# Optimization experiments

Measured on AMD Instinct MI355X. Metric: run time of the kernel, lower is better.

## Reference

```python
import jax, jax.numpy as jnp
import numpy as np

B, S, D, H = 4, 2048, 1024, 16
HD = D // H

def setup_inputs() -> dict:
    key = jax.random.key(0)
    k1, k2, k3, k4, k5 = jax.random.split(key, 5)
    sc = 1.0 / np.sqrt(D)
    return {
        "x": jax.random.normal(k1, (B, S, D), dtype=jnp.float32),
        "w_qkv": jax.random.normal(k2, (D, 3 * D), dtype=jnp.float32) * sc,
        "b_qkv": jnp.zeros((3 * D,), dtype=jnp.float32),
        "w_proj": jax.random.normal(k3, (D, D), dtype=jnp.float32) * sc,
        "b_proj": jnp.zeros((D,), dtype=jnp.float32),
    }

def reference(x, w_qkv, b_qkv, w_proj, b_proj):
    bsz, seq_len, dim = x.shape
    qkv = x @ w_qkv + b_qkv                      # [B,S,3D]
    q, k, v = jnp.split(qkv, 3, axis=2)
    q = q.reshape(bsz, seq_len, H, HD).transpose(0, 2, 1, 3)  # [B,H,S,hd]
    k = k.reshape(bsz, seq_len, H, HD).transpose(0, 2, 1, 3)
    v = v.reshape(bsz, seq_len, H, HD).transpose(0, 2, 1, 3)
    att = jnp.einsum('bhqd,bhkd->bhqk', q, k) * (1.0 / np.sqrt(HD))
    causal = jnp.tril(jnp.ones((seq_len, seq_len), dtype=bool))
    att = jnp.where(causal[None, None], att, -jnp.inf)
    att = jax.nn.softmax(att, axis=-1)
    y = jnp.einsum('bhqk,bhkd->bhqd', att, v)
    y = y.transpose(0, 2, 1, 3).reshape(bsz, seq_len, dim)
    return y @ w_proj + b_proj
```

## Files before the change

kernel.cpp:

```cpp
#include <hip/hip_runtime.h>
#include <cstdint>
#include <cstddef>

typedef float  f32x4  __attribute__((ext_vector_type(4)));
typedef __bf16 bf16x8 __attribute__((ext_vector_type(8)));
typedef __bf16 bf16x4 __attribute__((ext_vector_type(4)));

#define DEVI static __device__ __forceinline__

DEVI f32x4 mfma_bf16(bf16x8 a, bf16x8 b, f32x4 c) {
  return __builtin_amdgcn_mfma_f32_16x16x32_bf16(a, b, c, 0, 0, 0);
}

DEVI void gload_lds16(const void* g, void* l) {
  __builtin_amdgcn_global_load_lds(
      (const __attribute__((address_space(1))) void*)g,
      (__attribute__((address_space(3))) void*)l, 16, 0, 0);
}

__global__ void k_cast_bf16(const float* __restrict__ src, __bf16* __restrict__ dst, int n4) {
  int i = blockIdx.x * blockDim.x + threadIdx.x;
  if (i < n4) {
    float4 v = reinterpret_cast<const float4*>(src)[i];
    bf16x4 r;
    r.x = (__bf16)v.x; r.y = (__bf16)v.y; r.z = (__bf16)v.z; r.w = (__bf16)v.w;
    reinterpret_cast<bf16x4*>(dst)[i] = r;
  }
}

__global__ void k_transpose_cast(const float* __restrict__ src, __bf16* __restrict__ dst,
                                 int R, int C) {
  __shared__ __bf16 tile[64][65];
  const int tx = threadIdx.x & 63, ty = threadIdx.x >> 6;
  const int r0 = blockIdx.y * 64, c0 = blockIdx.x * 64;
#pragma unroll
  for (int i = 0; i < 16; ++i) {
    int r = ty * 16 + i;
    tile[r][tx] = (__bf16)src[(size_t)(r0 + r) * C + c0 + tx];
  }
  __syncthreads();
#pragma unroll
  for (int i = 0; i < 16; ++i) {
    int c = ty * 16 + i;
    dst[(size_t)(c0 + c) * R + r0 + tx] = tile[tx][c];
  }
}

__global__ void k_transpose_v(const __bf16* __restrict__ qkv, __bf16* __restrict__ VT) {
  __shared__ __bf16 tile[64][65];
  const int tx = threadIdx.x & 63, ty = threadIdx.x >> 6;
  const int bh = blockIdx.y;
  const int b = bh >> 4, h = bh & 15;
  const int s0 = blockIdx.x * 64;
  const __bf16* src = qkv + (size_t)(b * 2048) * 3072 + 2048 + h * 64;
#pragma unroll
  for (int i = 0; i < 16; ++i) {
    int s = ty * 16 + i;
    tile[s][tx] = src[(size_t)(s0 + s) * 3072 + tx];
  }
  __syncthreads();
  __bf16* dst = VT + (size_t)bh * 64 * 2048;
#pragma unroll
  for (int i = 0; i < 16; ++i) {
    int d = ty * 16 + i;
    dst[(size_t)d * 2048 + s0 + tx] = tile[tx][d];
  }
}

template <int MODE>
__global__ __launch_bounds__(256, 2) void k_gemm_bt(
    const __bf16* __restrict__ A, const __bf16* __restrict__ Bt,
    const float* __restrict__ bias, void* __restrict__ Cv,
    int M, int N, int K, int nbx) {
  __shared__ __bf16 As[128 * 64];
  __shared__ __bf16 Bs[128 * 64];
  const int t = threadIdx.x;
  const int w = t >> 6, lane = t & 63;
  const int l15 = lane & 15, lg = lane >> 4;
  const int m0 = (blockIdx.x / nbx) * 128;
  const int n0 = (blockIdx.x % nbx) * 128;
  const int wr = w >> 1, wc = w & 1;
  const int lrow = lane >> 3, lslot = lane & 7;

  f32x4 acc[4][4] = {};

  const int nK = K >> 6;
  for (int kt = 0; kt < nK; ++kt) {
    const __bf16* Ab = A + (size_t)m0 * K + kt * 64;
    const __bf16* Bb = Bt + (size_t)n0 * K + kt * 64;
#pragma unroll
    for (int c = 0; c < 4; ++c) {
      int seg = w * 4 + c;
      int row = seg * 8 + lrow;
      int cb = (lslot ^ (row & 7)) << 4;
      gload_lds16((const char*)(Ab + (size_t)row * K) + cb, (char*)As + seg * 1024);
      gload_lds16((const char*)(Bb + (size_t)row * K) + cb, (char*)Bs + seg * 1024);
    }
    __syncthreads();
#pragma unroll
    for (int ks = 0; ks < 2; ++ks) {
      bf16x8 af[4], bfr[4];
      const int cb = ks * 64 + (lg << 4);
#pragma unroll
      for (int m = 0; m < 4; ++m) {
        int row = wr * 64 + m * 16 + l15;
        af[m] = *(const bf16x8*)((const char*)As + row * 128 + (cb ^ ((row & 7) << 4)));
      }
#pragma unroll
      for (int n = 0; n < 4; ++n) {
        int row = wc * 64 + n * 16 + l15;
        bfr[n] = *(const bf16x8*)((const char*)Bs + row * 128 + (cb ^ ((row & 7) << 4)));
      }
#pragma unroll
      for (int m = 0; m < 4; ++m)
#pragma unroll
        for (int n = 0; n < 4; ++n)
          acc[m][n] = mfma_bf16(af[m], bfr[n], acc[m][n]);
    }
    __syncthreads();
  }

#pragma unroll
  for (int n = 0; n < 4; ++n) {
    const int gcol = n0 + wc * 64 + n * 16 + l15;
    const float bv = bias ? bias[gcol] : 0.0f;
#pragma unroll
    for (int m = 0; m < 4; ++m) {
      const int grow = m0 + wr * 64 + m * 16 + (lg << 2);
#pragma unroll
      for (int r = 0; r < 4; ++r) {
        float v = acc[m][n][r] + bv;
        if (MODE == 0)
          ((__bf16*)Cv)[(size_t)(grow + r) * N + gcol] = (__bf16)v;
        else
          ((float*)Cv)[(size_t)(grow + r) * N + gcol] = v;
      }
    }
  }
}

__global__ __launch_bounds__(512, 2) void k_attn(
    const __bf16* __restrict__ qkv,
    const __bf16* __restrict__ VT,
    __bf16* __restrict__ Y) {
  __shared__ __bf16 kbuf[2][64 * 64];
  __shared__ __bf16 vbuf[2][64 * 64];
  __shared__ __bf16 p_lds[8][1024];
  const int t = threadIdx.x, w = t >> 6, lane = t & 63;
  const int l15 = lane & 15, lg = lane >> 4;
  const int bid = blockIdx.x;
  const int qt = 15 - (bid >> 6);
  const int bh = bid & 63;
  const int b = bh >> 4, h = bh & 15;
  const int q0 = qt * 128;
  const int nkv = 2 * qt + 2;
  const float SCL = 0.125f * 1.44269504f;

  const size_t qrow = (size_t)(b * 2048 + q0 + w * 16 + l15);
  const bf16x8 qf0 = *(const bf16x8*)(qkv + qrow * 3072 + h * 64 + lg * 8);
  const bf16x8 qf1 = *(const bf16x8*)(qkv + qrow * 3072 + h * 64 + 32 + lg * 8);

  const __bf16* kg = qkv + (size_t)(b * 2048) * 3072 + 1024 + h * 64;
  const __bf16* vg = VT + (size_t)bh * 64 * 2048;

  const int srow = t >> 3, sslot = t & 7;
  const int sb = (sslot ^ (srow & 7)) << 4;
  auto stage = [&](int bi, int kvi) {
    gload_lds16((const char*)(kg + (size_t)(kvi * 64 + srow) * 3072) + sb,
                (char*)kbuf[bi] + w * 1024);
    gload_lds16((const char*)(vg + (size_t)srow * 2048 + kvi * 64) + sb,
                (char*)vbuf[bi] + w * 1024);
  };

  f32x4 o[4] = {};
  float mr = -1e30f, lr = 0.0f;
  __bf16* pl = &p_lds[w][0];

  stage(0, 0);
  asm volatile("s_waitcnt vmcnt(0)" ::: "memory");
  __syncthreads();

  for (int kv = 0; kv < nkv; ++kv) {
    if (kv + 1 < nkv) stage((kv + 1) & 1, kv + 1);
    const char* kb = (const char*)kbuf[kv & 1];
    const char* vb = (const char*)vbuf[kv & 1];

    f32x4 s[4] = {};
    __builtin_amdgcn_s_setprio(1);
#pragma unroll
    for (int nb = 0; nb < 4; ++nb) {
      int row = nb * 16 + l15;
      int sw = (row & 7) << 4;
      bf16x8 k0 = *(const bf16x8*)(kb + row * 128 + ((lg * 16) ^ sw));
      bf16x8 k1 = *(const bf16x8*)(kb + row * 128 + ((64 + lg * 16) ^ sw));
      s[nb] = mfma_bf16(k0, qf0, s[nb]);
      s[nb] = mfma_bf16(k1, qf1, s[nb]);
    }
    __builtin_amdgcn_s_setprio(0);

    if (((kv + 1) << 6) > q0 + w * 16) {
      const int qg = q0 + w * 16 + l15;
#pragma unroll
      for (int nb = 0; nb < 4; ++nb)
#pragma unroll
        for (int r = 0; r < 4; ++r)
          if (kv * 64 + nb * 16 + lg * 4 + r > qg) s[nb][r] = -1e30f;
    }

    float pm = -3e38f;
#pragma unroll
    for (int nb = 0; nb < 4; ++nb)
      pm = fmaxf(pm, fmaxf(fmaxf(s[nb][0], s[nb][1]), fmaxf(s[nb][2], s[nb][3])));
    pm = fmaxf(pm, __shfl_xor(pm, 16));
    pm = fmaxf(pm, __shfl_xor(pm, 32));
    pm *= SCL;

    if (!__all(pm <= mr + 8.0f)) {
      float nm = fmaxf(mr, pm);
      float alpha = __builtin_amdgcn_exp2f(mr - nm);
      lr *= alpha;
      mr = nm;
#pragma unroll
      for (int r = 0; r < 4; ++r) {
        float aO = __shfl(alpha, lg * 4 + r);
        o[0][r] *= aO; o[1][r] *= aO; o[2][r] *= aO; o[3][r] *= aO;
      }
    }

    float ps = 0.0f;
    bf16x4 pk[4];
#pragma unroll
    for (int nb = 0; nb < 4; ++nb) {
      f32x4 pe;
#pragma unroll
      for (int r = 0; r < 4; ++r)
        pe[r] = __builtin_amdgcn_exp2f(fmaf(s[nb][r], SCL, -mr));
      ps += (pe[0] + pe[1]) + (pe[2] + pe[3]);
      pk[nb][0] = (__bf16)pe[0]; pk[nb][1] = (__bf16)pe[1];
      pk[nb][2] = (__bf16)pe[2]; pk[nb][3] = (__bf16)pe[3];
    }
    ps += __shfl_xor(ps, 16);
    ps += __shfl_xor(ps, 32);
    lr += ps;

    {
      const int rowb = l15 * 128;
      const int sw = (l15 & 7) << 4;
#pragma unroll
      for (int nb = 0; nb < 4; ++nb) {
        int cb = (nb * 32 + lg * 8) ^ sw;
        *(bf16x4*)((char*)pl + rowb + cb) = pk[nb];
      }
    }
    asm volatile("s_waitcnt lgkmcnt(0)" ::: "memory");
    bf16x8 pf0, pf1;
    {
      const int rowb = l15 * 128;
      const int sw = (l15 & 7) << 4;
      pf0 = *(const bf16x8*)((const char*)pl + rowb + ((lg << 4) ^ sw));
      pf1 = *(const bf16x8*)((const char*)pl + rowb + ((64 + (lg << 4)) ^ sw));
    }
    __builtin_amdgcn_s_setprio(1);
#pragma unroll
    for (int nb = 0; nb < 4; ++nb) {
      int row = nb * 16 + l15;
      int sw = (row & 7) << 4;
      bf16x8 v0 = *(const bf16x8*)(vb + row * 128 + ((lg * 16) ^ sw));
      bf16x8 v1 = *(const bf16x8*)(vb + row * 128 + ((64 + lg * 16) ^ sw));
      o[nb] = mfma_bf16(pf0, v0, o[nb]);
      o[nb] = mfma_bf16(pf1, v1, o[nb]);
    }
    __builtin_amdgcn_s_setprio(0);
    asm volatile("s_waitcnt vmcnt(0)" ::: "memory");
    __syncthreads();
  }

  float lO[4];
#pragma unroll
  for (int r = 0; r < 4; ++r) lO[r] = __shfl(lr, lg * 4 + r);
#pragma unroll
  for (int nb = 0; nb < 4; ++nb)
#pragma unroll
    for (int r = 0; r < 4; ++r) {
      float v = o[nb][r] / lO[r];
      size_t row = (size_t)(b * 2048 + q0 + w * 16 + lg * 4 + r);
      Y[row * 1024 + h * 64 + nb * 16 + l15] = (__bf16)v;
    }
}

extern "C" void kernel_launch(void* const* d_in, const int* in_sizes, int n_in,
                              void* d_out, int out_size, void* d_ws, size_t ws_size,
                              hipStream_t stream) {
  const float* x      = (const float*)d_in[0];
  const float* w_qkv  = (const float*)d_in[1];
  const float* b_qkv  = (const float*)d_in[2];
  const float* w_proj = (const float*)d_in[3];
  const float* b_proj = (const float*)d_in[4];
  float* out = (float*)d_out;

  char* ws = (char*)d_ws;
  const size_t MB = 1024 * 1024;
  __bf16* xb     = (__bf16*)(ws);
  __bf16* wqkvT  = (__bf16*)(ws + 16 * MB);
  __bf16* wprojT = (__bf16*)(ws + 22 * MB);
  __bf16* qkv    = (__bf16*)(ws + 24 * MB);
  __bf16* VT     = (__bf16*)(ws + 72 * MB);
  __bf16* Y      = (__bf16*)(ws + 88 * MB);

  k_cast_bf16<<<8192, 256, 0, stream>>>(x, xb, 8192 * 1024 / 4);
  k_transpose_cast<<<dim3(48, 16), 256, 0, stream>>>(w_qkv, wqkvT, 1024, 3072);
  k_transpose_cast<<<dim3(16, 16), 256, 0, stream>>>(w_proj, wprojT, 1024, 1024);
  k_gemm_bt<0><<<dim3(64 * 24), 256, 0, stream>>>(xb, wqkvT, b_qkv, qkv, 8192, 3072, 1024, 24);
  k_transpose_v<<<dim3(32, 64), 256, 0, stream>>>(qkv, VT);
  k_attn<<<dim3(1024), 512, 0, stream>>>(qkv, VT, Y);
  k_gemm_bt<1><<<dim3(64 * 8), 256, 0, stream>>>(Y, wprojT, b_proj, out, 8192, 1024, 1024, 8);
}
```

Measured before the change: 178.2 us.

## Replace GEMM with 256x256-tile, 8-wave, double-buffered pipelined kernel

```diff
diff --git a/kernel.cpp b/kernel.cpp
--- a/kernel.cpp
+++ b/kernel.cpp
@@ -68,56 +68,127 @@
 }
 
 template <int MODE>
-__global__ __launch_bounds__(256, 2) void k_gemm_bt(
+__global__ __launch_bounds__(512, 2) void k_gemm8(
     const __bf16* __restrict__ A, const __bf16* __restrict__ Bt,
     const float* __restrict__ bias, void* __restrict__ Cv,
     int M, int N, int K, int nbx) {
-  __shared__ __bf16 As[128 * 64];
-  __shared__ __bf16 Bs[128 * 64];
+  __shared__ alignas(16) __bf16 Asl[2][2][256 * 32];
+  __shared__ alignas(16) __bf16 Bsl[2][2][256 * 32];
   const int t = threadIdx.x;
   const int w = t >> 6, lane = t & 63;
   const int l15 = lane & 15, lg = lane >> 4;
-  const int m0 = (blockIdx.x / nbx) * 128;
-  const int n0 = (blockIdx.x % nbx) * 128;
-  const int wr = w >> 1, wc = w & 1;
-  const int lrow = lane >> 3, lslot = lane & 7;
-
-  f32x4 acc[4][4] = {};
-
+  const int wr = w >> 2, wc = w & 3;
+
+  const int nwg = gridDim.x;
+  const int wgid = (blockIdx.x & 7) * (nwg >> 3) + (blockIdx.x >> 3);
+  const int m0 = (wgid / nbx) * 256;
+  const int n0 = (wgid % nbx) * 256;
+
+  const int lrow = lane & 15, lcol = lane >> 4;
+  const __bf16* pa = A + (size_t)(m0 + lrow) * K + lcol * 8;
+  const __bf16* pb = Bt + (size_t)(n0 + lrow) * K + lcol * 8;
+
+  auto stageA = [&](int buf, int kt, int kk) {
+    const __bf16* src = pa + (size_t)kt * 64 + kk * 32;
+    char* dst = (char*)&Asl[buf][kk][0];
+#pragma unroll
+    for (int i = 0; i < 2; ++i) {
+      const int st = w * 2 + i;
+      gload_lds16(src + (size_t)st * 16 * K, dst + st * 1024);
+    }
+  };
+  auto stageB = [&](int buf, int kt, int kk) {
+    const __bf16* src = pb + (size_t)kt * 64 + kk * 32;
+    char* dst = (char*)&Bsl[buf][kk][0];
+#pragma unroll
+    for (int i = 0; i < 2; ++i) {
+      const int st = w * 2 + i;
+      gload_lds16(src + (size_t)st * 16 * K, dst + st * 1024);
+    }
+  };
+
+  const int aoff = wr * 8192 + lg * 256 + l15 * 16;
+  const int boff = wc * 4096 + lg * 256 + l15 * 16;
+
+  f32x4 acc[8][4] = {};
   const int nK = K >> 6;
+
+  stageA(0, 0, 0); stageB(0, 0, 0);
+  stageA(0, 0, 1); stageB(0, 0, 1);
+  asm volatile("s_waitcnt vmcnt(4)" ::: "memory");
+  __builtin_amdgcn_s_barrier();
+
   for (int kt = 0; kt < nK; ++kt) {
-    const __bf16* Ab = A + (size_t)m0 * K + kt * 64;
-    const __bf16* Bb = Bt + (size_t)n0 * K + kt * 64;
-#pragma unroll
-    for (int c = 0; c < 4; ++c) {
-      int seg = w * 4 + c;
-      int row = seg * 8 + lrow;
-      int cb = (lslot ^ (row & 7)) << 4;
-      gload_lds16((const char*)(Ab + (size_t)row * K) + cb, (char*)As + seg * 1024);
-      gload_lds16((const char*)(Bb + (size_t)row * K) + cb, (char*)Bs + seg * 1024);
-    }
-    __syncthreads();
-#pragma unroll
-    for (int ks = 0; ks < 2; ++ks) {
-      bf16x8 af[4], bfr[4];
-      const int cb = ks * 64 + (lg << 4);
-#pragma unroll
-      for (int m = 0; m < 4; ++m) {
-        int row = wr * 64 + m * 16 + l15;
-        af[m] = *(const bf16x8*)((const char*)As + row * 128 + (cb ^ ((row & 7) << 4)));
-      }
-#pragma unroll
-      for (int n = 0; n < 4; ++n) {
-        int row = wc * 64 + n * 16 + l15;
-        bfr[n] = *(const bf16x8*)((const char*)Bs + row * 128 + (cb ^ ((row & 7) << 4)));
-      }
-#pragma unroll
-      for (int m = 0; m < 4; ++m)
-#pragma unroll
-        for (int n = 0; n < 4; ++n)
-          acc[m][n] = mfma_bf16(af[m], bfr[n], acc[m][n]);
-    }
-    __syncthreads();
+    const int buf = kt & 1, nbuf = buf ^ 1;
+    const bool pf = (kt + 1) < nK;
+    const char* a0 = (const char*)&Asl[buf][0][0];
+    const char* b0 = (const char*)&Bsl[buf][0][0];
+    const char* a1 = (const char*)&Asl[buf][1][0];
+    const char* b1 = (const char*)&Bsl[buf][1][0];
+    bf16x8 af[4], bfr[4];
+
+#pragma unroll
+    for (int m = 0; m < 4; ++m) af[m] = *(const bf16x8*)(a0 + aoff + m * 1024);
+#pragma unroll
+    for (int n = 0; n < 4; ++n) bfr[n] = *(const bf16x8*)(b0 + boff + n * 1024);
+    if (pf) stageA(nbuf, kt + 1, 0);
+    __builtin_amdgcn_s_barrier();
+    asm volatile("s_waitcnt lgkmcnt(0)" ::: "memory");
+    __builtin_amdgcn_s_setprio(1);
+#pragma unroll
+    for (int m = 0; m < 4; ++m)
+#pragma unroll
+      for (int n = 0; n < 4; ++n)
+        acc[m][n] = mfma_bf16(af[m], bfr[n], acc[m][n]);
+    __builtin_amdgcn_s_setprio(0);
+    __builtin_amdgcn_s_barrier();
+
+#pragma unroll
+    for (int m = 0; m < 4; ++m) af[m] = *(const bf16x8*)(a0 + aoff + (m + 4) * 1024);
+    if (pf) stageB(nbuf, kt + 1, 0);
+    __builtin_amdgcn_s_barrier();
+    asm volatile("s_waitcnt lgkmcnt(0)" ::: "memory");
+    __builtin_amdgcn_s_setprio(1);
+#pragma unroll
+    for (int m = 0; m < 4; ++m)
+#pragma unroll
+      for (int n = 0; n < 4; ++n)
+        acc[m + 4][n] = mfma_bf16(af[m], bfr[n], acc[m + 4][n]);
+    __builtin_amdgcn_s_setprio(0);
+    if (pf) asm volatile("s_waitcnt vmcnt(4)" ::: "memory");
+    else    asm volatile("s_waitcnt vmcnt(0)" ::: "memory");
+    __builtin_amdgcn_s_barrier();
+
+#pragma unroll
+    for (int m = 0; m < 4; ++m) af[m] = *(const bf16x8*)(a1 + aoff + m * 1024);
+#pragma unroll
+    for (int n = 0; n < 4; ++n) bfr[n] = *(const bf16x8*)(b1 + boff + n * 1024);
+    if (pf) stageA(nbuf, kt + 1, 1);
+    __builtin_amdgcn_s_barrier();
+    asm volatile("s_waitcnt lgkmcnt(0)" ::: "memory");
+    __builtin_amdgcn_s_setprio(1);
+#pragma unroll
+    for (int m = 0; m < 4; ++m)
+#pragma unroll
+      for (int n = 0; n < 4; ++n)
+        acc[m][n] = mfma_bf16(af[m], bfr[n], acc[m][n]);
+    __builtin_amdgcn_s_setprio(0);
+    __builtin_amdgcn_s_barrier();
+
+#pragma unroll
+    for (int m = 0; m < 4; ++m) af[m] = *(const bf16x8*)(a1 + aoff + (m + 4) * 1024);
+    if (pf) stageB(nbuf, kt + 1, 1);
+    __builtin_amdgcn_s_barrier();
+    asm volatile("s_waitcnt lgkmcnt(0)" ::: "memory");
+    __builtin_amdgcn_s_setprio(1);
+#pragma unroll
+    for (int m = 0; m < 4; ++m)
+#pragma unroll
+      for (int n = 0; n < 4; ++n)
+        acc[m + 4][n] = mfma_bf16(af[m], bfr[n], acc[m + 4][n]);
+    __builtin_amdgcn_s_setprio(0);
+    if (pf) asm volatile("s_waitcnt vmcnt(4)" ::: "memory");
+    __builtin_amdgcn_s_barrier();
   }
 
 #pragma unroll
@@ -125,8 +196,8 @@
     const int gcol = n0 + wc * 64 + n * 16 + l15;
     const float bv = bias ? bias[gcol] : 0.0f;
 #pragma unroll
-    for (int m = 0; m < 4; ++m) {
-      const int grow = m0 + wr * 64 + m * 16 + (lg << 2);
+    for (int m = 0; m < 8; ++m) {
+      const int grow = m0 + wr * 128 + m * 16 + (lg << 2);
 #pragma unroll
       for (int r = 0; r < 4; ++r) {
         float v = acc[m][n][r] + bv;
@@ -310,8 +381,8 @@
   k_cast_bf16<<<8192, 256, 0, stream>>>(x, xb, 8192 * 1024 / 4);
   k_transpose_cast<<<dim3(48, 16), 256, 0, stream>>>(w_qkv, wqkvT, 1024, 3072);
   k_transpose_cast<<<dim3(16, 16), 256, 0, stream>>>(w_proj, wprojT, 1024, 1024);
-  k_gemm_bt<0><<<dim3(64 * 24), 256, 0, stream>>>(xb, wqkvT, b_qkv, qkv, 8192, 3072, 1024, 24);
+  k_gemm8<0><<<dim3(384), 512, 0, stream>>>(xb, wqkvT, b_qkv, qkv, 8192, 3072, 1024, 12);
   k_transpose_v<<<dim3(32, 64), 256, 0, stream>>>(qkv, VT);
   k_attn<<<dim3(1024), 512, 0, stream>>>(qkv, VT, Y);
-  k_gemm_bt<1><<<dim3(64 * 8), 256, 0, stream>>>(Y, wprojT, b_proj, out, 8192, 1024, 1024, 8);
-}
+  k_gemm8<1><<<dim3(128), 512, 0, stream>>>(Y, wprojT, b_proj, out, 8192, 1024, 1024, 4);
+}
```

After: 212.4 us. 19.2% more time.
